# Performance work log

Hardware: AMD Instinct MI355X
Metric: run time of the kernel (lower is better)

The kernel has to match this reference:

```python
import jax, jax.numpy as jnp
import numpy as np

B, S, D = 4, 2048, 1024
MULT = 4
INNER = MULT * D
E = 4          # n_expert
K = 1          # top-k
ALPHA = 0.5


def setup_inputs() -> dict:
    key = jax.random.key(0)
    ks = jax.random.split(key, 8)
    std = 0.02
    x = jax.random.normal(ks[0], (B, S, D), jnp.float32)
    W1 = jax.random.normal(ks[1], (D, INNER), jnp.float32) * std
    b1 = jnp.zeros((INNER,), jnp.float32)
    W2 = jax.random.normal(ks[2], (INNER, D), jnp.float32) * std
    b2 = jnp.zeros((D,), jnp.float32)
    Wg = jax.random.normal(ks[3], (D, E), jnp.float32) * std
    ew1 = jax.random.normal(ks[4], (E, D, INNER), jnp.float32) * std
    ew3 = jax.random.normal(ks[5], (E, D, INNER), jnp.float32) * std
    ew2 = jax.random.normal(ks[6], (E, INNER, D), jnp.float32) * std
    return {"x": x, "W1": W1, "b1": b1, "W2": W2, "b2": b2,
            "Wg": Wg, "ew1": ew1, "ew3": ew3, "ew2": ew2}


def reference(x, W1, b1, W2, b2, Wg, ew1, ew3, ew2):
    # Dense branch: Linear -> GELU (exact, torch default) -> Linear
    y_dense = jax.nn.gelu(x @ W1 + b1, approximate=False) @ W2 + b2

    # MoE branch: top-k softmax routing, SwiGLU experts
    logits = x @ Wg                                   # [B,S,E]
    probs = jax.nn.softmax(logits, axis=-1)
    topv, topi = jax.lax.top_k(probs, K)              # [B,S,K]
    gates = topv / jnp.sum(topv, axis=-1, keepdims=True)  # renormalize top-k
    onehot = jax.nn.one_hot(topi, E, dtype=x.dtype)   # [B,S,K,E]
    combine = jnp.sum(gates[..., None] * onehot, axis=-2)  # [B,S,E]

    y_moe = jnp.zeros_like(x)
    for e in range(E):  # small fixed expert count
        h = jax.nn.silu(x @ ew1[e]) * (x @ ew3[e])    # [B,S,INNER]
        y_moe = y_moe + combine[..., e:e + 1] * (h @ ew2[e])

    # Load-balancing aux loss: E * sum_e f_e * P_e
    frac = jnp.mean(jnp.sum(onehot, axis=-2), axis=(0, 1)) / K  # [E]
    pmean = jnp.mean(probs, axis=(0, 1))                        # [E]
    aux = E * jnp.sum(frac * pmean)

    y = ALPHA * y_dense + (1.0 - ALPHA) * y_moe
    return (y, aux)
```

## Files before the change

### kernel.cpp

```cpp
#include <hip/hip_runtime.h>
#include <hip/hip_bf16.h>


static constexpr int MT = 8192;
static constexpr int DD = 1024;
static constexpr int DI = 4096;

typedef float f32x4 __attribute__((ext_vector_type(4)));
typedef __bf16 bf16x8 __attribute__((ext_vector_type(8)));
typedef unsigned short u16;

__device__ __forceinline__ u16 f2bf(float f) {
    union { __hip_bfloat16 b; u16 u; } v;
    v.b = __float2bfloat16(f);
    return v.u;
}

__device__ __forceinline__ void gload_lds16(const void* g, void* l) {
    __builtin_amdgcn_global_load_lds(
        (const __attribute__((address_space(1))) void*)g,
        (__attribute__((address_space(3))) void*)l, 16, 0, 0);
}

__device__ __forceinline__ float gelu_f(float v) {
    return 0.5f * v * (1.0f + erff(v * 0.70710678118654752f));
}
__device__ __forceinline__ float silu_f(float v) {
    return v / (1.0f + expf(-v));
}

__global__ void __launch_bounds__(256) transpose_cvt(
    const float* __restrict__ src, u16* __restrict__ dst, int K, int N) {
    __shared__ u16 t[64][72];
    const float* s = src + (size_t)blockIdx.z * K * N;
    u16* d = dst + (size_t)blockIdx.z * K * N;
    int n0 = blockIdx.x * 64, k0 = blockIdx.y * 64;
    int tid = threadIdx.x;
    int c = tid & 15;
    int r = tid >> 4;
#pragma unroll
    for (int p = 0; p < 4; ++p) {
        int k = r + p * 16;
        float4 v = *(const float4*)(s + (size_t)(k0 + k) * N + n0 + c * 4);
        t[c * 4 + 0][k] = f2bf(v.x);
        t[c * 4 + 1][k] = f2bf(v.y);
        t[c * 4 + 2][k] = f2bf(v.z);
        t[c * 4 + 3][k] = f2bf(v.w);
    }
    __syncthreads();
    int n = tid >> 2, kc = (tid & 3) * 16;
    const uint4* p0 = (const uint4*)&t[n][kc];
    uint4 a = p0[0], b = p0[1];
    uint4* o = (uint4*)(d + (size_t)(n0 + n) * K + k0 + kc);
    o[0] = a; o[1] = b;
}

__global__ void __launch_bounds__(256) gate_kernel(
    const float* __restrict__ x, const float* __restrict__ Wg,
    float* __restrict__ psum_blk, int* __restrict__ expertA) {
    int w = threadIdx.x >> 6, l = threadIdx.x & 63;
    int t = blockIdx.x * 4 + w;
    const float* xr = x + (size_t)t * DD;
    double a0 = 0, a1 = 0, a2 = 0, a3 = 0;
#pragma unroll
    for (int i = 0; i < 4; ++i) {
        int k = i * 256 + l * 4;
        float4 xv = *(const float4*)(xr + k);
        float4 w0 = *(const float4*)(Wg + (size_t)(k + 0) * 4);
        float4 w1 = *(const float4*)(Wg + (size_t)(k + 1) * 4);
        float4 w2 = *(const float4*)(Wg + (size_t)(k + 2) * 4);
        float4 w3 = *(const float4*)(Wg + (size_t)(k + 3) * 4);
        a0 += (double)xv.x * w0.x + (double)xv.y * w1.x + (double)xv.z * w2.x + (double)xv.w * w3.x;
        a1 += (double)xv.x * w0.y + (double)xv.y * w1.y + (double)xv.z * w2.y + (double)xv.w * w3.y;
        a2 += (double)xv.x * w0.z + (double)xv.y * w1.z + (double)xv.z * w2.z + (double)xv.w * w3.z;
        a3 += (double)xv.x * w0.w + (double)xv.y * w1.w + (double)xv.z * w2.w + (double)xv.w * w3.w;
    }
#pragma unroll
    for (int o = 32; o; o >>= 1) {
        a0 += __shfl_down(a0, o); a1 += __shfl_down(a1, o);
        a2 += __shfl_down(a2, o); a3 += __shfl_down(a3, o);
    }
    __shared__ float wps[4][4];
    if (l == 0) {
        double lg[4] = {a0, a1, a2, a3};
        int best = 0;
#pragma unroll
        for (int e = 1; e < 4; ++e) if (lg[e] > lg[best]) best = e;
        double m = lg[best], s = 0, p[4];
#pragma unroll
        for (int e = 0; e < 4; ++e) { p[e] = exp(lg[e] - m); s += p[e]; }
#pragma unroll
        for (int e = 0; e < 4; ++e) wps[w][e] = (float)(p[e] / s);
        expertA[t] = best;
    }
    __syncthreads();
    if (threadIdx.x < 4)
        psum_blk[blockIdx.x * 4 + threadIdx.x] =
            wps[0][threadIdx.x] + wps[1][threadIdx.x] + wps[2][threadIdx.x] + wps[3][threadIdx.x];
}

__global__ void __launch_bounds__(1024) build_lists(
    const int* __restrict__ expertA, const float* __restrict__ psum_blk,
    int* __restrict__ dstArr, int* __restrict__ rev,
    int* __restrict__ offsets, float* __restrict__ auxOut) {
    __shared__ int sc[4][1024];
    __shared__ float fs[1024];
    __shared__ float psum_s[4];
    __shared__ int tot_s[4], off_s[4];
    int tid = threadIdx.x;
    int le[8]; int c[4] = {0, 0, 0, 0};
#pragma unroll
    for (int i = 0; i < 8; ++i) { int e = expertA[tid * 8 + i]; le[i] = e; c[e]++; }
#pragma unroll
    for (int e = 0; e < 4; ++e) sc[e][tid] = c[e];
    __syncthreads();
    for (int o = 1; o < 1024; o <<= 1) {
        int v[4];
#pragma unroll
        for (int e = 0; e < 4; ++e) v[e] = (tid >= o) ? sc[e][tid - o] : 0;
        __syncthreads();
#pragma unroll
        for (int e = 0; e < 4; ++e) if (tid >= o) sc[e][tid] += v[e];
        __syncthreads();
    }
    if (tid == 0) {
        int o = 0;
#pragma unroll
        for (int e = 0; e < 4; ++e) {
            tot_s[e] = sc[e][1023]; off_s[e] = o; offsets[e] = o; o += tot_s[e];
        }
        offsets[4] = o;
    }
    __syncthreads();
    int base[4];
#pragma unroll
    for (int e = 0; e < 4; ++e) base[e] = off_s[e] + sc[e][tid] - c[e];
#pragma unroll
    for (int i = 0; i < 8; ++i) {
        int e = le[i]; int d = base[e]++; int t = tid * 8 + i;
        dstArr[t] = d; rev[d] = t;
    }
    float ps[4];
#pragma unroll
    for (int e = 0; e < 4; ++e)
        ps[e] = psum_blk[(2 * tid) * 4 + e] + psum_blk[(2 * tid + 1) * 4 + e];
    for (int e = 0; e < 4; ++e) {
        fs[tid] = ps[e]; __syncthreads();
        for (int o = 512; o; o >>= 1) { if (tid < o) fs[tid] += fs[tid + o]; __syncthreads(); }
        if (tid == 0) psum_s[e] = fs[0];
        __syncthreads();
    }
    if (tid == 0) {
        float a = 0;
#pragma unroll
        for (int e = 0; e < 4; ++e)
            a += ((float)tot_s[e] * (1.f / 8192.f)) * (psum_s[e] * (1.f / 8192.f));
        auxOut[0] = 4.f * a;
    }
}

__global__ void __launch_bounds__(256) gather_kernel(
    const float* __restrict__ x, const int* __restrict__ dstArr,
    u16* __restrict__ xb, u16* __restrict__ xg) {
    int w = threadIdx.x >> 6, l = threadIdx.x & 63;
    int t = blockIdx.x * 4 + w;
    int dst = dstArr[t];
    const float* xr = x + (size_t)t * DD;
#pragma unroll
    for (int i = 0; i < 4; ++i) {
        int k = i * 256 + l * 4;
        float4 v = *(const float4*)(xr + k);
        ushort4 u;
        u.x = f2bf(v.x); u.y = f2bf(v.y); u.z = f2bf(v.z); u.w = f2bf(v.w);
        *(ushort4*)(xb + (size_t)t * DD + k) = u;
        *(ushort4*)(xg + (size_t)dst * DD + k) = u;
    }
}

template <int MODE>
__global__ void __launch_bounds__(256) gemm_kernel(
    const u16* __restrict__ A, const u16* __restrict__ Bw,
    const u16* __restrict__ Bw2, const float* __restrict__ bias,
    u16* __restrict__ outB, float* __restrict__ outF,
    const int* __restrict__ offsets, const int* __restrict__ rev,
    int N, int K) {
    constexpr int BM = 128;
    constexpr int WN = (MODE == 2) ? 32 : 64;
    constexpr int FRN = (MODE == 2) ? 2 : 4;
    constexpr int BN = (MODE == 2) ? 64 : 128;
    __shared__ u16 ldsA[BM * 32];
    __shared__ u16 ldsB[128 * 32];
    int tid = threadIdx.x, w = tid >> 6, l = tid & 63;
    int wr = w >> 1, wc = w & 1;
    int rowBase, rowsValid;
    const u16* B1 = Bw;
    const u16* B2 = Bw2;
    if constexpr (MODE == 2 || MODE == 3) {
        int e = blockIdx.z;
        int off = offsets[e];
        int cnt = offsets[e + 1] - off;
        int rb = blockIdx.y;
        if (rb * BM >= cnt) return;
        rowBase = off + rb * BM;
        rowsValid = cnt - rb * BM;
        if (rowsValid > BM) rowsValid = BM;
        size_t wOff = (size_t)e * DI * DD;
        B1 = Bw + wOff;
        if constexpr (MODE == 2) B2 = Bw2 + wOff;
    } else {
        rowBase = blockIdx.y * BM;
        rowsValid = BM;
    }
    int colBase = blockIdx.x * BN;

    f32x4 acc[4][FRN];
    f32x4 acc2[4][FRN];
#pragma unroll
    for (int m = 0; m < 4; ++m)
#pragma unroll
        for (int n = 0; n < FRN; ++n) {
            acc[m][n] = (f32x4){0.f, 0.f, 0.f, 0.f};
            if constexpr (MODE == 2) acc2[m][n] = (f32x4){0.f, 0.f, 0.f, 0.f};
        }

    int lr = l & 15, lg = l >> 4;
    int ar = l >> 2, ac = (l & 3) * 8;

    const int nkt = K >> 5;
    for (int kt = 0; kt < nkt; ++kt) {
        int k0 = kt << 5;
        {
            const u16* ga = A + (size_t)(rowBase + w * 32 + ar) * K + k0 + ac;
            gload_lds16(ga, &ldsA[(w * 32) * 32]);
            gload_lds16(ga + (size_t)16 * K, &ldsA[(w * 32 + 16) * 32]);
        }
        if constexpr (MODE == 2) {
            const u16* bsrc = (w < 2) ? B1 : B2;
            int nrel = (w & 1) * 32;
            const u16* gb = bsrc + (size_t)(colBase + nrel + ar) * K + k0 + ac;
            int lo = ((w < 2 ? 0 : 64) + nrel) * 32;
            gload_lds16(gb, &ldsB[lo]);
            gload_lds16(gb + (size_t)16 * K, &ldsB[lo + 16 * 32]);
        } else {
            const u16* gb = B1 + (size_t)(colBase + w * 32 + ar) * K + k0 + ac;
            gload_lds16(gb, &ldsB[(w * 32) * 32]);
            gload_lds16(gb + (size_t)16 * K, &ldsB[(w * 32 + 16) * 32]);
        }
        __syncthreads();
        bf16x8 af[4], bfr[FRN], bfr2[FRN];
#pragma unroll
        for (int m = 0; m < 4; ++m)
            af[m] = *(const bf16x8*)&ldsA[(wr * 64 + m * 16 + lr) * 32 + lg * 8];
#pragma unroll
        for (int n = 0; n < FRN; ++n) {
            bfr[n] = *(const bf16x8*)&ldsB[(wc * WN + n * 16 + lr) * 32 + lg * 8];
            if constexpr (MODE == 2)
                bfr2[n] = *(const bf16x8*)&ldsB[(64 + wc * WN + n * 16 + lr) * 32 + lg * 8];
        }
#pragma unroll
        for (int m = 0; m < 4; ++m)
#pragma unroll
            for (int n = 0; n < FRN; ++n) {
                acc[m][n] = __builtin_amdgcn_mfma_f32_16x16x32_bf16(bfr[n], af[m], acc[m][n], 0, 0, 0);
                if constexpr (MODE == 2)
                    acc2[m][n] = __builtin_amdgcn_mfma_f32_16x16x32_bf16(bfr2[n], af[m], acc2[m][n], 0, 0, 0);
            }
        __syncthreads();
    }

#pragma unroll
    for (int m = 0; m < 4; ++m) {
        int rloc = wr * 64 + m * 16 + lr;
        if ((MODE == 2 || MODE == 3) && rloc >= rowsValid) continue;
        size_t grow = (size_t)(rowBase + rloc);
#pragma unroll
        for (int n = 0; n < FRN; ++n) {
            int ncol = colBase + wc * WN + n * 16 + lg * 4;
            f32x4 v = acc[m][n];
            if constexpr (MODE == 0) {
                f32x4 bb = *(const f32x4*)(bias + ncol);
                ushort4 u;
                u.x = f2bf(gelu_f(v[0] + bb[0]));
                u.y = f2bf(gelu_f(v[1] + bb[1]));
                u.z = f2bf(gelu_f(v[2] + bb[2]));
                u.w = f2bf(gelu_f(v[3] + bb[3]));
                *(ushort4*)(outB + grow * N + ncol) = u;
            } else if constexpr (MODE == 1) {
                f32x4 bb = *(const f32x4*)(bias + ncol);
                f32x4 r;
#pragma unroll
                for (int j = 0; j < 4; ++j) r[j] = 0.5f * (v[j] + bb[j]);
                *(f32x4*)(outF + grow * N + ncol) = r;
            } else if constexpr (MODE == 2) {
                f32x4 v3 = acc2[m][n];
                ushort4 u;
                u.x = f2bf(silu_f(v[0]) * v3[0]);
                u.y = f2bf(silu_f(v[1]) * v3[1]);
                u.z = f2bf(silu_f(v[2]) * v3[2]);
                u.w = f2bf(silu_f(v[3]) * v3[3]);
                *(ushort4*)(outB + grow * N + ncol) = u;
            } else {
                int tok = rev[grow];
                f32x4* p = (f32x4*)(outF + (size_t)tok * N + ncol);
                f32x4 o = *p;
#pragma unroll
                for (int j = 0; j < 4; ++j) o[j] += 0.5f * v[j];
                *p = o;
            }
        }
    }
}

extern "C" void kernel_launch(void* const* d_in, const int* in_sizes, int n_in,
                              void* d_out, int out_size, void* d_ws, size_t ws_size,
                              hipStream_t stream) {
    const float* x   = (const float*)d_in[0];
    const float* W1  = (const float*)d_in[1];
    const float* b1  = (const float*)d_in[2];
    const float* W2  = (const float*)d_in[3];
    const float* b2  = (const float*)d_in[4];
    const float* Wg  = (const float*)d_in[5];
    const float* ew1 = (const float*)d_in[6];
    const float* ew3 = (const float*)d_in[7];
    const float* ew2 = (const float*)d_in[8];
    float* y = (float*)d_out;
    float* auxOut = y + (size_t)MT * DD;

    char* ws = (char*)d_ws;
    size_t off = 0;
    auto take = [&](size_t b) -> void* {
        void* p = ws + off;
        off += (b + 255) & ~(size_t)255;
        return p;
    };
    u16* W1t  = (u16*)take((size_t)DI * DD * 2);
    u16* W2t  = (u16*)take((size_t)DI * DD * 2);
    u16* ew1t = (u16*)take((size_t)4 * DI * DD * 2);
    u16* ew3t = (u16*)take((size_t)4 * DI * DD * 2);
    u16* ew2t = (u16*)take((size_t)4 * DI * DD * 2);
    u16* xb   = (u16*)take((size_t)MT * DD * 2);
    u16* xg   = (u16*)take((size_t)MT * DD * 2);
    u16* hd   = (u16*)take((size_t)(MT + 130) * DI * 2);
    int* expertA  = (int*)take(MT * 4);
    int* dstArr   = (int*)take(MT * 4);
    int* revA     = (int*)take(MT * 4);
    float* psum_blk = (float*)take(2048 * 4 * 4);
    int* offsets  = (int*)take(64);
    u16* hg = hd;

    if (ws_size < off) return;

    dim3 blk(256);
    transpose_cvt<<<dim3(64, 16, 1), blk, 0, stream>>>(W1,  W1t,  DD, DI);
    transpose_cvt<<<dim3(64, 16, 4), blk, 0, stream>>>(ew1, ew1t, DD, DI);
    transpose_cvt<<<dim3(64, 16, 4), blk, 0, stream>>>(ew3, ew3t, DD, DI);
    transpose_cvt<<<dim3(16, 64, 1), blk, 0, stream>>>(W2,  W2t,  DI, DD);
    transpose_cvt<<<dim3(16, 64, 4), blk, 0, stream>>>(ew2, ew2t, DI, DD);
    gate_kernel<<<2048, 256, 0, stream>>>(x, Wg, psum_blk, expertA);
    build_lists<<<1, 1024, 0, stream>>>(expertA, psum_blk, dstArr, revA, offsets, auxOut);
    gather_kernel<<<2048, 256, 0, stream>>>(x, dstArr, xb, xg);
    gemm_kernel<0><<<dim3(DI / 128, MT / 128, 1), blk, 0, stream>>>(
        xb, W1t, nullptr, b1, hd, nullptr, nullptr, nullptr, DI, DD);
    gemm_kernel<1><<<dim3(DD / 128, MT / 128, 1), blk, 0, stream>>>(
        hd, W2t, nullptr, b2, nullptr, y, nullptr, nullptr, DD, DI);
    gemm_kernel<2><<<dim3(DI / 64, MT / 128, 4), blk, 0, stream>>>(
        xg, ew1t, ew3t, nullptr, hg, nullptr, offsets, nullptr, DI, DD);
    gemm_kernel<3><<<dim3(DD / 128, MT / 128, 4), blk, 0, stream>>>(
        hg, ew2t, nullptr, nullptr, nullptr, y, offsets, revA, DD, DI);
}
```

Measured before the change: 671.6 us.

## Rewrite GEMMs as 512-thread double-buffered 256-row tiles with interleaved expert weights

Replaces the 128x128 single-buffered GEMM with a 512-thread kernel that uses 256-row tiles, a double-buffered LDS pipeline over 64-wide K steps, an XOR swizzle against bank conflicts, and explicit barrier/waitcnt scheduling with setprio around the MFMA bursts. The w1/w3 expert weights are packed into one interleaved buffer in 32-row groups, so the SwiGLU GEMM streams a single B operand and pairs accumulators in the epilogue. The intent is to overlap global loads with MFMA work and raise arithmetic intensity per tile. In exchange it uses more LDS and registers, needs padding on the gathered buffers for over-reads, and wastes more rows on ragged expert tails.

```diff
diff --git a/kernel.cpp b/kernel.cpp
--- a/kernel.cpp
+++ b/kernel.cpp
@@ -29,11 +29,16 @@
     return v / (1.0f + expf(-v));
 }
 
+#define FENCE() asm volatile("" ::: "memory")
+#define BARRIER() do { FENCE(); __builtin_amdgcn_s_barrier(); FENCE(); } while (0)
+#define WAIT_LGKM0() asm volatile("s_waitcnt lgkmcnt(0)" ::: "memory")
+
 __global__ void __launch_bounds__(256) transpose_cvt(
-    const float* __restrict__ src, u16* __restrict__ dst, int K, int N) {
+    const float* __restrict__ src, u16* __restrict__ dst, int K, int N,
+    int pack, int packOff, size_t srcMatStride, size_t dstMatStride) {
     __shared__ u16 t[64][72];
-    const float* s = src + (size_t)blockIdx.z * K * N;
-    u16* d = dst + (size_t)blockIdx.z * K * N;
+    const float* s = src + (size_t)blockIdx.z * srcMatStride;
+    u16* d = dst + (size_t)blockIdx.z * dstMatStride;
     int n0 = blockIdx.x * 64, k0 = blockIdx.y * 64;
     int tid = threadIdx.x;
     int c = tid & 15;
@@ -51,7 +56,9 @@
     int n = tid >> 2, kc = (tid & 3) * 16;
     const uint4* p0 = (const uint4*)&t[n][kc];
     uint4 a = p0[0], b = p0[1];
-    uint4* o = (uint4*)(d + (size_t)(n0 + n) * K + k0 + kc);
+    int gn = n0 + n;
+    int dr = pack ? ((gn >> 5) * 64 + (gn & 31) + packOff) : gn;
+    uint4* o = (uint4*)(d + (size_t)dr * K + k0 + kc);
     o[0] = a; o[1] = b;
 }
 
@@ -177,138 +184,175 @@
     }
 }
 
-template <int MODE>
-__global__ void __launch_bounds__(256) gemm_kernel(
+template <int MODE, int NF>
+__global__ void __launch_bounds__(512, 2) gemm8(
     const u16* __restrict__ A, const u16* __restrict__ Bw,
-    const u16* __restrict__ Bw2, const float* __restrict__ bias,
+    const float* __restrict__ bias,
     u16* __restrict__ outB, float* __restrict__ outF,
     const int* __restrict__ offsets, const int* __restrict__ rev,
     int N, int K) {
-    constexpr int BM = 128;
-    constexpr int WN = (MODE == 2) ? 32 : 64;
-    constexpr int FRN = (MODE == 2) ? 2 : 4;
-    constexpr int BN = (MODE == 2) ? 64 : 128;
-    __shared__ u16 ldsA[BM * 32];
-    __shared__ u16 ldsB[128 * 32];
-    int tid = threadIdx.x, w = tid >> 6, l = tid & 63;
-    int wr = w >> 1, wc = w & 1;
-    int rowBase, rowsValid;
-    const u16* B1 = Bw;
-    const u16* B2 = Bw2;
-    if constexpr (MODE == 2 || MODE == 3) {
+    constexpr int BN   = NF * 64;
+    constexpr int WCW  = NF * 16;
+    constexpr int AELT = 2 * 256 * 32;
+    constexpr int BUFE = AELT + 2 * BN * 32;
+    constexpr int NIB  = NF / 2;
+    __shared__ u16 lds[2 * BUFE];
+
+    const int tid = threadIdx.x;
+    const int w = tid >> 6, l = tid & 63;
+    const int lr = l & 15, lg = l >> 4;
+    const int wr = w >> 2, wc = w & 3;
+
+    int rowBase, rowsValid = 256;
+    const u16* Bp = Bw;
+    if constexpr (MODE >= 2) {
         int e = blockIdx.z;
-        int off = offsets[e];
-        int cnt = offsets[e + 1] - off;
-        int rb = blockIdx.y;
-        if (rb * BM >= cnt) return;
-        rowBase = off + rb * BM;
-        rowsValid = cnt - rb * BM;
-        if (rowsValid > BM) rowsValid = BM;
-        size_t wOff = (size_t)e * DI * DD;
-        B1 = Bw + wOff;
-        if constexpr (MODE == 2) B2 = Bw2 + wOff;
+        int off = offsets[e], cnt = offsets[e + 1] - off;
+        if ((int)blockIdx.y * 256 >= cnt) return;
+        rowBase = off + blockIdx.y * 256;
+        rowsValid = cnt - (int)blockIdx.y * 256;
+        if (rowsValid > 256) rowsValid = 256;
+        Bp = Bw + (size_t)e * ((size_t)(MODE == 2 ? 2 : 1) * DD * DI);
     } else {
-        rowBase = blockIdx.y * BM;
-        rowsValid = BM;
-    }
-    int colBase = blockIdx.x * BN;
-
-    f32x4 acc[4][FRN];
-    f32x4 acc2[4][FRN];
-#pragma unroll
-    for (int m = 0; m < 4; ++m)
-#pragma unroll
-        for (int n = 0; n < FRN; ++n) {
-            acc[m][n] = (f32x4){0.f, 0.f, 0.f, 0.f};
-            if constexpr (MODE == 2) acc2[m][n] = (f32x4){0.f, 0.f, 0.f, 0.f};
+        rowBase = blockIdx.y * 256;
+    }
+    const int colBase = blockIdx.x * BN;
+    const int NT = K >> 6;
+
+    auto stageA = [&](int kt, int b, int ks) {
+        const int kk = (kt << 6) + (ks << 5);
+#pragma unroll
+        for (int i = 0; i < 2; ++i) {
+            int o = ((w << 1) + i) * 512 + (l << 3);
+            int o2 = o ^ (((o >> 8) & 1) << 4);
+            gload_lds16(A + (size_t)(rowBase + (o2 >> 5)) * K + kk + (o2 & 31),
+                        &lds[b * BUFE + ks * 8192 + ((w << 1) + i) * 512]);
         }
-
-    int lr = l & 15, lg = l >> 4;
-    int ar = l >> 2, ac = (l & 3) * 8;
-
-    const int nkt = K >> 5;
-    for (int kt = 0; kt < nkt; ++kt) {
-        int k0 = kt << 5;
-        {
-            const u16* ga = A + (size_t)(rowBase + w * 32 + ar) * K + k0 + ac;
-            gload_lds16(ga, &ldsA[(w * 32) * 32]);
-            gload_lds16(ga + (size_t)16 * K, &ldsA[(w * 32 + 16) * 32]);
+    };
+    auto stageB = [&](int kt, int b, int ks) {
+        const int kk = (kt << 6) + (ks << 5);
+#pragma unroll
+        for (int i = 0; i < NIB; ++i) {
+            int o = (w * NIB + i) * 512 + (l << 3);
+            int o2 = o ^ (((o >> 8) & 1) << 4);
+            gload_lds16(Bp + (size_t)(colBase + (o2 >> 5)) * K + kk + (o2 & 31),
+                        &lds[b * BUFE + AELT + ks * (BN * 32) + (w * NIB + i) * 512]);
         }
+    };
+
+#define WAIT_VMB() do { \
+    if constexpr (NF == 4) asm volatile("s_waitcnt vmcnt(4)" ::: "memory"); \
+    else                   asm volatile("s_waitcnt vmcnt(3)" ::: "memory"); \
+} while (0)
+
+#define READBF(b_, ks_) do { \
+    _Pragma("unroll") \
+    for (int n = 0; n < NF; ++n) { \
+        int e_ = (wc * WCW + n * 16 + lr) * 32 + lg * 8; \
+        e_ ^= ((e_ >> 8) & 1) << 4; \
+        bf[n] = *(const bf16x8*)&lds[(b_) * BUFE + AELT + (ks_) * (BN * 32) + e_]; \
+    } \
+} while (0)
+
+#define READAF(b_, ks_, mq_) do { \
+    _Pragma("unroll") \
+    for (int m = 0; m < 4; ++m) { \
+        int e_ = (wr * 128 + ((mq_) * 4 + m) * 16 + lr) * 32 + lg * 8; \
+        e_ ^= ((e_ >> 8) & 1) << 4; \
+        af[m] = *(const bf16x8*)&lds[(b_) * BUFE + (ks_) * 8192 + e_]; \
+    } \
+} while (0)
+
+#define DOMFMA(mq_) do { \
+    __builtin_amdgcn_s_setprio(1); \
+    _Pragma("unroll") \
+    for (int m = 0; m < 4; ++m) \
+    _Pragma("unroll") \
+    for (int n = 0; n < NF; ++n) \
+        acc[(mq_) * 4 + m][n] = __builtin_amdgcn_mfma_f32_16x16x32_bf16( \
+            bf[n], af[m], acc[(mq_) * 4 + m][n], 0, 0, 0); \
+    __builtin_amdgcn_s_setprio(0); \
+} while (0)
+
+    f32x4 acc[8][NF];
+#pragma unroll
+    for (int m = 0; m < 8; ++m)
+#pragma unroll
+        for (int n = 0; n < NF; ++n) acc[m][n] = (f32x4){0.f, 0.f, 0.f, 0.f};
+    bf16x8 af[4], bf[NF];
+
+    stageA(0, 0, 0); stageB(0, 0, 0); stageA(0, 0, 1); stageB(0, 0, 1);
+    stageA(1, 1, 0); stageB(1, 1, 0);
+    WAIT_VMB();
+    BARRIER();
+
+    for (int t = 0; t < NT; ++t) {
+        const int cb = t & 1, nb = cb ^ 1;
+        const int tp1 = (t + 1 < NT) ? t + 1 : NT - 1;
+        const int tp2 = (t + 2 < NT) ? t + 2 : NT - 1;
+        READBF(cb, 0); READAF(cb, 0, 0); stageA(tp1, nb, 1);
+        BARRIER(); WAIT_LGKM0(); DOMFMA(0); BARRIER();
+        READAF(cb, 0, 1); stageB(tp1, nb, 1);
+        BARRIER(); WAIT_LGKM0(); DOMFMA(1); BARRIER();
+        READBF(cb, 1); READAF(cb, 1, 0); stageA(tp2, cb, 0);
+        BARRIER(); WAIT_LGKM0(); DOMFMA(0); BARRIER();
+        READAF(cb, 1, 1); stageB(tp2, cb, 0);
+        BARRIER(); WAIT_LGKM0(); DOMFMA(1);
+        WAIT_VMB();
+        BARRIER();
+    }
+
+#pragma unroll
+    for (int m = 0; m < 8; ++m) {
+        int rloc = wr * 128 + m * 16 + lr;
+        if (MODE >= 2 && rloc >= rowsValid) continue;
+        size_t grow = (size_t)(rowBase + rloc);
         if constexpr (MODE == 2) {
-            const u16* bsrc = (w < 2) ? B1 : B2;
-            int nrel = (w & 1) * 32;
-            const u16* gb = bsrc + (size_t)(colBase + nrel + ar) * K + k0 + ac;
-            int lo = ((w < 2 ? 0 : 64) + nrel) * 32;
-            gload_lds16(gb, &ldsB[lo]);
-            gload_lds16(gb + (size_t)16 * K, &ldsB[lo + 16 * 32]);
+#pragma unroll
+            for (int n = 0; n < 2; ++n) {
+                int col = (colBase >> 1) + wc * 32 + n * 16 + lg * 4;
+                f32x4 v1 = acc[m][n], v3 = acc[m][n + 2];
+                ushort4 u;
+                u.x = f2bf(silu_f(v1[0]) * v3[0]);
+                u.y = f2bf(silu_f(v1[1]) * v3[1]);
+                u.z = f2bf(silu_f(v1[2]) * v3[2]);
+                u.w = f2bf(silu_f(v1[3]) * v3[3]);
+                *(ushort4*)(outB + grow * N + col) = u;
+            }
         } else {
-            const u16* gb = B1 + (size_t)(colBase + w * 32 + ar) * K + k0 + ac;
-            gload_lds16(gb, &ldsB[(w * 32) * 32]);
-            gload_lds16(gb + (size_t)16 * K, &ldsB[(w * 32 + 16) * 32]);
-        }
-        __syncthreads();
-        bf16x8 af[4], bfr[FRN], bfr2[FRN];
-#pragma unroll
-        for (int m = 0; m < 4; ++m)
-            af[m] = *(const bf16x8*)&ldsA[(wr * 64 + m * 16 + lr) * 32 + lg * 8];
-#pragma unroll
-        for (int n = 0; n < FRN; ++n) {
-            bfr[n] = *(const bf16x8*)&ldsB[(wc * WN + n * 16 + lr) * 32 + lg * 8];
-            if constexpr (MODE == 2)
-                bfr2[n] = *(const bf16x8*)&ldsB[(64 + wc * WN + n * 16 + lr) * 32 + lg * 8];
-        }
-#pragma unroll
-        for (int m = 0; m < 4; ++m)
-#pragma unroll
-            for (int n = 0; n < FRN; ++n) {
-                acc[m][n] = __builtin_amdgcn_mfma_f32_16x16x32_bf16(bfr[n], af[m], acc[m][n], 0, 0, 0);
-                if constexpr (MODE == 2)
-                    acc2[m][n] = __builtin_amdgcn_mfma_f32_16x16x32_bf16(bfr2[n], af[m], acc2[m][n], 0, 0, 0);
-            }
-        __syncthreads();
-    }
-
-#pragma unroll
-    for (int m = 0; m < 4; ++m) {
-        int rloc = wr * 64 + m * 16 + lr;
-        if ((MODE == 2 || MODE == 3) && rloc >= rowsValid) continue;
-        size_t grow = (size_t)(rowBase + rloc);
-#pragma unroll
-        for (int n = 0; n < FRN; ++n) {
-            int ncol = colBase + wc * WN + n * 16 + lg * 4;
-            f32x4 v = acc[m][n];
-            if constexpr (MODE == 0) {
-                f32x4 bb = *(const f32x4*)(bias + ncol);
-                ushort4 u;
-                u.x = f2bf(gelu_f(v[0] + bb[0]));
-                u.y = f2bf(gelu_f(v[1] + bb[1]));
-                u.z = f2bf(gelu_f(v[2] + bb[2]));
-                u.w = f2bf(gelu_f(v[3] + bb[3]));
-                *(ushort4*)(outB + grow * N + ncol) = u;
-            } else if constexpr (MODE == 1) {
-                f32x4 bb = *(const f32x4*)(bias + ncol);
-                f32x4 r;
-#pragma unroll
-                for (int j = 0; j < 4; ++j) r[j] = 0.5f * (v[j] + bb[j]);
-                *(f32x4*)(outF + grow * N + ncol) = r;
-            } else if constexpr (MODE == 2) {
-                f32x4 v3 = acc2[m][n];
-                ushort4 u;
-                u.x = f2bf(silu_f(v[0]) * v3[0]);
-                u.y = f2bf(silu_f(v[1]) * v3[1]);
-                u.z = f2bf(silu_f(v[2]) * v3[2]);
-                u.w = f2bf(silu_f(v[3]) * v3[3]);
-                *(ushort4*)(outB + grow * N + ncol) = u;
-            } else {
-                int tok = rev[grow];
-                f32x4* p = (f32x4*)(outF + (size_t)tok * N + ncol);
-                f32x4 o = *p;
-#pragma unroll
-                for (int j = 0; j < 4; ++j) o[j] += 0.5f * v[j];
-                *p = o;
+#pragma unroll
+            for (int n = 0; n < NF; ++n) {
+                int col = colBase + wc * WCW + n * 16 + lg * 4;
+                f32x4 v = acc[m][n];
+                if constexpr (MODE == 0) {
+                    f32x4 bb = *(const f32x4*)(bias + col);
+                    ushort4 u;
+                    u.x = f2bf(gelu_f(v[0] + bb[0]));
+                    u.y = f2bf(gelu_f(v[1] + bb[1]));
+                    u.z = f2bf(gelu_f(v[2] + bb[2]));
+                    u.w = f2bf(gelu_f(v[3] + bb[3]));
+                    *(ushort4*)(outB + grow * N + col) = u;
+                } else if constexpr (MODE == 1) {
+                    f32x4 bb = *(const f32x4*)(bias + col);
+                    f32x4 r;
+#pragma unroll
+                    for (int j = 0; j < 4; ++j) r[j] = 0.5f * (v[j] + bb[j]);
+                    *(f32x4*)(outF + grow * N + col) = r;
+                } else {
+                    int tok = rev[grow];
+                    f32x4* p = (f32x4*)(outF + (size_t)tok * N + col);
+                    f32x4 o = *p;
+#pragma unroll
+                    for (int j = 0; j < 4; ++j) o[j] += 0.5f * v[j];
+                    *p = o;
+                }
             }
         }
     }
+#undef WAIT_VMB
+#undef READBF
+#undef READAF
+#undef DOMFMA
 }
 
 extern "C" void kernel_launch(void* const* d_in, const int* in_sizes, int n_in,
@@ -333,14 +377,13 @@
         off += (b + 255) & ~(size_t)255;
         return p;
     };
-    u16* W1t  = (u16*)take((size_t)DI * DD * 2);
-    u16* W2t  = (u16*)take((size_t)DI * DD * 2);
-    u16* ew1t = (u16*)take((size_t)4 * DI * DD * 2);
-    u16* ew3t = (u16*)take((size_t)4 * DI * DD * 2);
-    u16* ew2t = (u16*)take((size_t)4 * DI * DD * 2);
-    u16* xb   = (u16*)take((size_t)MT * DD * 2);
-    u16* xg   = (u16*)take((size_t)MT * DD * 2);
-    u16* hd   = (u16*)take((size_t)(MT + 130) * DI * 2);
+    u16* W1t   = (u16*)take((size_t)DI * DD * 2);
+    u16* W2t   = (u16*)take((size_t)DI * DD * 2);
+    u16* ew13t = (u16*)take((size_t)4 * 2 * DI * DD * 2);
+    u16* ew2t  = (u16*)take((size_t)4 * DI * DD * 2);
+    u16* xb    = (u16*)take((size_t)MT * DD * 2);
+    u16* xg    = (u16*)take((size_t)(MT + 256) * DD * 2);
+    u16* hd    = (u16*)take((size_t)(MT + 256) * DI * 2);
     int* expertA  = (int*)take(MT * 4);
     int* dstArr   = (int*)take(MT * 4);
     int* revA     = (int*)take(MT * 4);
@@ -351,20 +394,20 @@
     if (ws_size < off) return;
 
     dim3 blk(256);
-    transpose_cvt<<<dim3(64, 16, 1), blk, 0, stream>>>(W1,  W1t,  DD, DI);
-    transpose_cvt<<<dim3(64, 16, 4), blk, 0, stream>>>(ew1, ew1t, DD, DI);
-    transpose_cvt<<<dim3(64, 16, 4), blk, 0, stream>>>(ew3, ew3t, DD, DI);
-    transpose_cvt<<<dim3(16, 64, 1), blk, 0, stream>>>(W2,  W2t,  DI, DD);
-    transpose_cvt<<<dim3(16, 64, 4), blk, 0, stream>>>(ew2, ew2t, DI, DD);
+    transpose_cvt<<<dim3(64, 16, 1), blk, 0, stream>>>(W1,  W1t,  DD, DI, 0, 0,  (size_t)DD * DI, (size_t)DD * DI);
+    transpose_cvt<<<dim3(64, 16, 4), blk, 0, stream>>>(ew1, ew13t, DD, DI, 1, 0,  (size_t)DD * DI, (size_t)2 * DD * DI);
+    transpose_cvt<<<dim3(64, 16, 4), blk, 0, stream>>>(ew3, ew13t, DD, DI, 1, 32, (size_t)DD * DI, (size_t)2 * DD * DI);
+    transpose_cvt<<<dim3(16, 64, 1), blk, 0, stream>>>(W2,  W2t,  DI, DD, 0, 0,  (size_t)DD * DI, (size_t)DD * DI);
+    transpose_cvt<<<dim3(16, 64, 4), blk, 0, stream>>>(ew2, ew2t, DI, DD, 0, 0,  (size_t)DD * DI, (size_t)DD * DI);
     gate_kernel<<<2048, 256, 0, stream>>>(x, Wg, psum_blk, expertA);
     build_lists<<<1, 1024, 0, stream>>>(expertA, psum_blk, dstArr, revA, offsets, auxOut);
     gather_kernel<<<2048, 256, 0, stream>>>(x, dstArr, xb, xg);
-    gemm_kernel<0><<<dim3(DI / 128, MT / 128, 1), blk, 0, stream>>>(
-        xb, W1t, nullptr, b1, hd, nullptr, nullptr, nullptr, DI, DD);
-    gemm_kernel<1><<<dim3(DD / 128, MT / 128, 1), blk, 0, stream>>>(
-        hd, W2t, nullptr, b2, nullptr, y, nullptr, nullptr, DD, DI);
-    gemm_kernel<2><<<dim3(DI / 64, MT / 128, 4), blk, 0, stream>>>(
-        xg, ew1t, ew3t, nullptr, hg, nullptr, offsets, nullptr, DI, DD);
-    gemm_kernel<3><<<dim3(DD / 128, MT / 128, 4), blk, 0, stream>>>(
-        hg, ew2t, nullptr, nullptr, nullptr, y, offsets, revA, DD, DI);
-}
+    gemm8<0, 4><<<dim3(DI / 256, MT / 256), dim3(512), 0, stream>>>(
+        xb, W1t, b1, hd, nullptr, nullptr, nullptr, DI, DD);
+    gemm8<1, 2><<<dim3(DD / 128, MT / 256), dim3(512), 0, stream>>>(
+        hd, W2t, b2, nullptr, y, nullptr, nullptr, DD, DI);
+    gemm8<2, 4><<<dim3(2 * DI / 256, MT / 256, 4), dim3(512), 0, stream>>>(
+        xg, ew13t, nullptr, hg, nullptr, offsets, nullptr, DI, DD);
+    gemm8<3, 2><<<dim3(DD / 128, MT / 256, 4), dim3(512), 0, stream>>>(
+        hg, ew2t, nullptr, nullptr, y, offsets, revA, DD, DI);
+}
```

New measurement: 641.1 us. 4.5% less time.
